# Kernel optimization log

Measured on AMD Instinct MI355X. Metric: run time of the kernel, lower is better.

The kernel has to match this reference:

```python
import jax, jax.numpy as jnp
import numpy as np

B, T, D, H, E = 4, 1024, 1024, 4096, 8
TOP_K = 2

def setup_inputs() -> dict:
    key = jax.random.key(0)
    ks = jax.random.split(key, 7)
    s = 0.02
    return {
        "x": jax.random.normal(ks[0], (B, T, D), dtype=jnp.float32),
        "gate_w": jax.random.normal(ks[1], (D, E), dtype=jnp.float32) * s,
        "gate_b": jnp.zeros((E,), dtype=jnp.float32),
        "w1": jax.random.normal(ks[2], (E, D, H), dtype=jnp.float32) * s,
        "b1": jnp.zeros((E, H), dtype=jnp.float32),
        "w2": jax.random.normal(ks[3], (E, H, D), dtype=jnp.float32) * s,
        "b2": jnp.zeros((E, D), dtype=jnp.float32),
    }

def reference(x, gate_w, gate_b, w1, b1, w2, b2):
    # gate: [B,T,E] softmax over experts
    gate_scores = jax.nn.softmax(x @ gate_w + gate_b, axis=-1)
    top_g, top_i = jax.lax.top_k(gate_scores, TOP_K)  # [B,T,K]
    # dense all-expert FFN (faithful to original: every expert on every token)
    h = jax.nn.relu(jnp.einsum("btd,edh->bteh", x, w1) + b1)   # [B,T,E,H]
    expert_out = jnp.einsum("bteh,ehd->bted", h, w2) + b2      # [B,T,E,D]
    # gather top-k expert outputs and combine with gate weights
    sel = jnp.take_along_axis(expert_out, top_i[..., None], axis=2)  # [B,T,K,D]
    return jnp.sum(top_g[..., None] * sel, axis=2)  # [B,T,D]
```

## Files before the change

### kernel.cpp

```cpp
#include <hip/hip_runtime.h>

#define MTOK   4096
#define DD     1024
#define HH     4096
#define EE     8
#define NPAIRS 8192
#define PADM   128

typedef __attribute__((ext_vector_type(8))) _Float16 half8;
typedef __attribute__((ext_vector_type(4))) _Float16 half4;
typedef __attribute__((ext_vector_type(4))) float    f32x4;

__device__ __forceinline__ void gload_lds16(const void* g, void* l) {
  __builtin_amdgcn_global_load_lds((const __attribute__((address_space(1))) void*)g,
                                   (__attribute__((address_space(3))) void*)l,
                                   16, 0, 0);
}

__global__ void k_init(int* counts) {
  if (threadIdx.x < EE) counts[threadIdx.x] = 0;
}

__global__ __launch_bounds__(256) void k_gate(
    const float* __restrict__ x, const float* __restrict__ gw,
    const float* __restrict__ gb, int* __restrict__ counts,
    int* __restrict__ topi, float* __restrict__ topg)
{
  __shared__ float W[EE][DD];
  int tid = threadIdx.x;
  for (int i = tid; i < DD*EE/4; i += 256) {
    f32x4 v = ((const f32x4*)gw)[i];
    int flat = i*4;
#pragma unroll
    for (int j = 0; j < 4; ++j) { int f = flat + j; W[f & 7][f >> 3] = v[j]; }
  }
  __syncthreads();
  int w = tid >> 6, lane = tid & 63;
  int t = blockIdx.x*4 + w;
  float acc[EE];
#pragma unroll
  for (int e = 0; e < EE; ++e) acc[e] = 0.f;
  const float* xr = x + (size_t)t*DD;
  for (int kk = 0; kk < DD/64; ++kk) {
    int k = kk*64 + lane;
    float xv = xr[k];
#pragma unroll
    for (int e = 0; e < EE; ++e) acc[e] += xv * W[e][k];
  }
#pragma unroll
  for (int off = 32; off >= 1; off >>= 1) {
#pragma unroll
    for (int e = 0; e < EE; ++e) acc[e] += __shfl_down(acc[e], off, 64);
  }
  if (lane == 0) {
#pragma unroll
    for (int e = 0; e < EE; ++e) acc[e] += gb[e];
    int i0 = 0;
#pragma unroll
    for (int e = 1; e < EE; ++e) if (acc[e] > acc[i0]) i0 = e;
    int i1 = (i0 == 0) ? 1 : 0;
#pragma unroll
    for (int e = 0; e < EE; ++e)
      if (e != i0 && e != i1 && acc[e] > acc[i1]) i1 = e;
    float m = acc[i0], s = 0.f, ex[EE];
#pragma unroll
    for (int e = 0; e < EE; ++e) { ex[e] = expf(acc[e] - m); s += ex[e]; }
    float inv = 1.f / s;
    topi[2*t] = i0;  topi[2*t+1] = i1;
    topg[2*t] = ex[i0]*inv;  topg[2*t+1] = ex[i1]*inv;
    atomicAdd(&counts[i0], 1);
    atomicAdd(&counts[i1], 1);
  }
}

__global__ void k_prefix(const int* counts, int* offs, int* cursor) {
  if (threadIdx.x == 0) {
    int s = 0;
    for (int e = 0; e < EE; ++e) { offs[e] = s; cursor[e] = s; s += counts[e]; }
    offs[EE] = s;
  }
}

__global__ void k_build(const int* __restrict__ topi, const float* __restrict__ topg,
                        int* __restrict__ cursor, int* __restrict__ tok_of,
                        float* __restrict__ gate_of, int* __restrict__ slot_of)
{
  int t = blockIdx.x*blockDim.x + threadIdx.x;
  if (t >= MTOK) return;
#pragma unroll
  for (int k = 0; k < 2; ++k) {
    int e = topi[2*t+k];
    int pos = atomicAdd(&cursor[e], 1);
    tok_of[pos]  = t;
    gate_of[pos] = topg[2*t+k];
    slot_of[2*t+k] = pos;
  }
}

__global__ __launch_bounds__(256) void k_gather(
    const float* __restrict__ x, const int* __restrict__ tok_of,
    _Float16* __restrict__ xg)
{
  int p = blockIdx.x;
  int t = tok_of[p];
  const f32x4* src = (const f32x4*)(x + (size_t)t*DD);
  half4* dst = (half4*)(xg + (size_t)p*DD);
  int i = threadIdx.x;
  f32x4 v = src[i];
  half4 h = { (_Float16)v[0], (_Float16)v[1], (_Float16)v[2], (_Float16)v[3] };
  dst[i] = h;
}

__global__ __launch_bounds__(256) void k_transpose(
    const float* __restrict__ in, _Float16* __restrict__ out, int Kd, int Nd)
{
  __shared__ _Float16 tile[64][72];
  int e = blockIdx.z;
  int n0 = blockIdx.x*64, k0 = blockIdx.y*64;
  int tid = threadIdx.x;
  int rq = tid >> 4, c4 = (tid & 15)*4;
  const float* src = in + (size_t)e*Kd*Nd;
#pragma unroll
  for (int rr = 0; rr < 4; ++rr) {
    int kr = rr*16 + rq;
    f32x4 v = *(const f32x4*)(src + (size_t)(k0+kr)*Nd + n0 + c4);
#pragma unroll
    for (int j = 0; j < 4; ++j) tile[c4+j][kr] = (_Float16)v[j];
  }
  __syncthreads();
  _Float16* dst = out + (size_t)e*Nd*Kd;
#pragma unroll
  for (int rr = 0; rr < 4; ++rr) {
    int nr = rr*16 + rq;
    half4 h;
#pragma unroll
    for (int j = 0; j < 4; ++j) h[j] = tile[nr][c4+j];
    *(half4*)(dst + (size_t)(n0+nr)*Kd + k0 + c4) = h;
  }
}

template<int EPI>
__global__ __launch_bounds__(256) void k_gemm(
    const _Float16* __restrict__ A, const _Float16* __restrict__ Bt,
    const float* __restrict__ bias, const int* __restrict__ offs,
    const int* __restrict__ counts, const float* __restrict__ gate_of,
    _Float16* __restrict__ Ch, float* __restrict__ Cf, int Kdim, int Ndim)
{
  int e = blockIdx.z;
  int cnt = counts[e];
  int m0 = blockIdx.y*128;
  if (m0 >= cnt) return;
  int n0 = blockIdx.x*128;
  int row_base = offs[e] + m0;

  __shared__ alignas(16) _Float16 lsA[128*64];
  __shared__ alignas(16) _Float16 lsB[128*64];

  int tid = threadIdx.x, w = tid >> 6, lane = tid & 63;
  int wr = w >> 1, wc = w & 1;

  f32x4 acc[4][4];
#pragma unroll
  for (int ni = 0; ni < 4; ++ni) {
    float bv = bias[(size_t)e*Ndim + n0 + wc*64 + ni*16 + (lane & 15)];
#pragma unroll
    for (int mi = 0; mi < 4; ++mi) acc[mi][ni] = (f32x4){bv, bv, bv, bv};
  }

  int arow[4], acol[4];
#pragma unroll
  for (int i = 0; i < 4; ++i) {
    int o = w*4096 + i*1024 + lane*16;
    int row = o >> 7;
    int chunk = (o >> 4) & 7;
    arow[i] = row;
    acol[i] = (chunk ^ (row & 7)) * 8;
  }

  const _Float16* Arow = A + (size_t)row_base*Kdim;
  const _Float16* Brow = Bt + ((size_t)e*Ndim + n0)*Kdim;

  for (int k0 = 0; k0 < Kdim; k0 += 64) {
#pragma unroll
    for (int i = 0; i < 4; ++i)
      gload_lds16(Arow + (size_t)arow[i]*Kdim + k0 + acol[i],
                  (char*)lsA + w*4096 + i*1024);
#pragma unroll
    for (int i = 0; i < 4; ++i)
      gload_lds16(Brow + (size_t)arow[i]*Kdim + k0 + acol[i],
                  (char*)lsB + w*4096 + i*1024);
    __syncthreads();
#pragma unroll
    for (int ks = 0; ks < 2; ++ks) {
      half8 af[4], bf[4];
#pragma unroll
      for (int mi = 0; mi < 4; ++mi) {
        int r = wr*64 + mi*16 + (lane & 15);
        int byt = (r*128 + ks*64 + ((lane >> 4) << 4)) ^ ((r & 7) << 4);
        af[mi] = *(const half8*)((const char*)lsA + byt);
      }
#pragma unroll
      for (int ni = 0; ni < 4; ++ni) {
        int r = wc*64 + ni*16 + (lane & 15);
        int byt = (r*128 + ks*64 + ((lane >> 4) << 4)) ^ ((r & 7) << 4);
        bf[ni] = *(const half8*)((const char*)lsB + byt);
      }
#pragma unroll
      for (int mi = 0; mi < 4; ++mi)
#pragma unroll
        for (int ni = 0; ni < 4; ++ni)
          acc[mi][ni] = __builtin_amdgcn_mfma_f32_16x16x32_f16(af[mi], bf[ni], acc[mi][ni], 0, 0, 0);
    }
    __syncthreads();
  }

#pragma unroll
  for (int mi = 0; mi < 4; ++mi) {
    int rl = wr*64 + mi*16 + ((lane >> 4) << 2);
#pragma unroll
    for (int ni = 0; ni < 4; ++ni) {
      int cl = n0 + wc*64 + ni*16 + (lane & 15);
#pragma unroll
      for (int r = 0; r < 4; ++r) {
        if (m0 + rl + r >= cnt) continue;
        size_t grow = (size_t)(row_base + rl + r);
        float v = acc[mi][ni][r];
        if (EPI == 0) Ch[grow*Ndim + cl] = (_Float16)fmaxf(v, 0.f);
        else          Cf[grow*Ndim + cl] = v * gate_of[grow];
      }
    }
  }
}

__global__ __launch_bounds__(256) void k_combine(
    const float* __restrict__ o2, const int* __restrict__ slot_of,
    float* __restrict__ out)
{
  int t = blockIdx.x;
  int s0 = slot_of[2*t], s1 = slot_of[2*t+1];
  const f32x4* a = (const f32x4*)(o2 + (size_t)s0*DD);
  const f32x4* b = (const f32x4*)(o2 + (size_t)s1*DD);
  f32x4* o = (f32x4*)(out + (size_t)t*DD);
  int i = threadIdx.x;
  o[i] = a[i] + b[i];
}

extern "C" void kernel_launch(void* const* d_in, const int* in_sizes, int n_in,
                              void* d_out, int out_size, void* d_ws, size_t ws_size,
                              hipStream_t stream)
{
  const float* x  = (const float*)d_in[0];
  const float* gw = (const float*)d_in[1];
  const float* gb = (const float*)d_in[2];
  const float* w1 = (const float*)d_in[3];
  const float* b1 = (const float*)d_in[4];
  const float* w2 = (const float*)d_in[5];
  const float* b2 = (const float*)d_in[6];
  float* out = (float*)d_out;
  char* ws = (char*)d_ws;

  size_t off = 0;
  auto alloc = [&](size_t b) {
    off = (off + 255) & ~(size_t)255;
    size_t o = off; off += b; return o;
  };
  int*   counts  = (int*)  (ws + alloc(EE*4));
  int*   offs    = (int*)  (ws + alloc((EE+1)*4));
  int*   cursor  = (int*)  (ws + alloc(EE*4));
  int*   topi    = (int*)  (ws + alloc((size_t)MTOK*2*4));
  float* topg    = (float*)(ws + alloc((size_t)MTOK*2*4));
  int*   tok_of  = (int*)  (ws + alloc((size_t)NPAIRS*4));
  float* gate_of = (float*)(ws + alloc((size_t)NPAIRS*4));
  int*   slot_of = (int*)  (ws + alloc((size_t)MTOK*2*4));
  _Float16* xg  = (_Float16*)(ws + alloc((size_t)(NPAIRS+PADM)*DD*2));
  _Float16* hb  = (_Float16*)(ws + alloc((size_t)(NPAIRS+PADM)*HH*2));
  _Float16* w1t = (_Float16*)(ws + alloc((size_t)EE*HH*DD*2));
  _Float16* w2t = (_Float16*)(ws + alloc((size_t)EE*DD*HH*2));
  float* o2 = (float*)w1t;

  k_init<<<1, 64, 0, stream>>>(counts);
  k_gate<<<MTOK/4, 256, 0, stream>>>(x, gw, gb, counts, topi, topg);
  k_prefix<<<1, 64, 0, stream>>>(counts, offs, cursor);
  k_build<<<MTOK/256, 256, 0, stream>>>(topi, topg, cursor, tok_of, gate_of, slot_of);
  k_gather<<<NPAIRS, 256, 0, stream>>>(x, tok_of, xg);
  k_transpose<<<dim3(HH/64, DD/64, EE), 256, 0, stream>>>(w1, w1t, DD, HH);
  k_transpose<<<dim3(DD/64, HH/64, EE), 256, 0, stream>>>(w2, w2t, HH, DD);
  k_gemm<0><<<dim3(HH/128, MTOK/128, EE), 256, 0, stream>>>(
      xg, w1t, b1, offs, counts, nullptr, hb, nullptr, DD, HH);
  k_gemm<1><<<dim3(DD/128, MTOK/128, EE), 256, 0, stream>>>(
      hb, w2t, b2, offs, counts, gate_of, nullptr, o2, HH, DD);
  k_combine<<<MTOK, 256, 0, stream>>>(o2, slot_of, out);
}
```

Measured before the change: 776.5 us.

## Double-buffer GEMM LDS, split-K second GEMM, XCD-aware block remap, staged epilogue

```diff
diff --git a/kernel.cpp b/kernel.cpp
--- a/kernel.cpp
+++ b/kernel.cpp
@@ -139,22 +139,34 @@
   }
 }
 
-template<int EPI>
+template<int EPI, int KS, int KD, int ND>
 __global__ __launch_bounds__(256) void k_gemm(
     const _Float16* __restrict__ A, const _Float16* __restrict__ Bt,
     const float* __restrict__ bias, const int* __restrict__ offs,
     const int* __restrict__ counts, const float* __restrict__ gate_of,
-    _Float16* __restrict__ Ch, float* __restrict__ Cf, int Kdim, int Ndim)
-{
-  int e = blockIdx.z;
+    _Float16* __restrict__ Ch, float* __restrict__ Cf)
+{
+  constexpr int NT = ND >> 7;
+  constexpr int MT = MTOK >> 7;
+  int total = NT * MT * EE * KS;
+  int lid = blockIdx.x;
+  int logical = (lid & 7) * (total >> 3) + (lid >> 3);
+  int n  = logical % NT;
+  int rem = logical / NT;
+  int m  = rem % MT;
+  int z  = rem / MT;
+  int e  = z / KS, ks = z % KS;
+
   int cnt = counts[e];
-  int m0 = blockIdx.y*128;
+  int m0 = m << 7;
   if (m0 >= cnt) return;
-  int n0 = blockIdx.x*128;
+  int n0 = n << 7;
   int row_base = offs[e] + m0;
-
-  __shared__ alignas(16) _Float16 lsA[128*64];
-  __shared__ alignas(16) _Float16 lsB[128*64];
+  constexpr int Kper = KD / KS;
+  int kbeg = ks * Kper;
+
+  constexpr int LSZ = (EPI == 1) ? (128*132*4) : 65536;
+  __shared__ alignas(16) char ls[LSZ];
 
   int tid = threadIdx.x, w = tid >> 6, lane = tid & 63;
   int wr = w >> 1, wc = w & 1;
@@ -162,7 +174,8 @@
   f32x4 acc[4][4];
 #pragma unroll
   for (int ni = 0; ni < 4; ++ni) {
-    float bv = bias[(size_t)e*Ndim + n0 + wc*64 + ni*16 + (lane & 15)];
+    float bv = (EPI == 0 || ks == 0)
+             ? bias[(size_t)e*ND + n0 + wc*64 + ni*16 + (lane & 15)] : 0.f;
 #pragma unroll
     for (int mi = 0; mi < 4; ++mi) acc[mi][ni] = (f32x4){bv, bv, bv, bv};
   }
@@ -177,33 +190,37 @@
     acol[i] = (chunk ^ (row & 7)) * 8;
   }
 
-  const _Float16* Arow = A + (size_t)row_base*Kdim;
-  const _Float16* Brow = Bt + ((size_t)e*Ndim + n0)*Kdim;
-
-  for (int k0 = 0; k0 < Kdim; k0 += 64) {
+  const _Float16* Arow = A + (size_t)row_base*KD + kbeg;
+  const _Float16* Brow = Bt + ((size_t)e*ND + n0)*KD + kbeg;
+
+  auto STAGE = [&](int buf, int k0) {
+    char* dA = ls + buf*16384;
+    char* dB = ls + 32768 + buf*16384;
 #pragma unroll
     for (int i = 0; i < 4; ++i)
-      gload_lds16(Arow + (size_t)arow[i]*Kdim + k0 + acol[i],
-                  (char*)lsA + w*4096 + i*1024);
+      gload_lds16(Arow + (size_t)arow[i]*KD + k0 + acol[i], dA + w*4096 + i*1024);
 #pragma unroll
     for (int i = 0; i < 4; ++i)
-      gload_lds16(Brow + (size_t)arow[i]*Kdim + k0 + acol[i],
-                  (char*)lsB + w*4096 + i*1024);
-    __syncthreads();
-#pragma unroll
-    for (int ks = 0; ks < 2; ++ks) {
+      gload_lds16(Brow + (size_t)arow[i]*KD + k0 + acol[i], dB + w*4096 + i*1024);
+  };
+
+  auto COMPUTE = [&](int buf) {
+    const char* sA = ls + buf*16384;
+    const char* sB = ls + 32768 + buf*16384;
+#pragma unroll
+    for (int ks2 = 0; ks2 < 2; ++ks2) {
       half8 af[4], bf[4];
 #pragma unroll
       for (int mi = 0; mi < 4; ++mi) {
         int r = wr*64 + mi*16 + (lane & 15);
-        int byt = (r*128 + ks*64 + ((lane >> 4) << 4)) ^ ((r & 7) << 4);
-        af[mi] = *(const half8*)((const char*)lsA + byt);
+        int byt = (r*128 + ks2*64 + ((lane >> 4) << 4)) ^ ((r & 7) << 4);
+        af[mi] = *(const half8*)(sA + byt);
       }
 #pragma unroll
       for (int ni = 0; ni < 4; ++ni) {
         int r = wc*64 + ni*16 + (lane & 15);
-        int byt = (r*128 + ks*64 + ((lane >> 4) << 4)) ^ ((r & 7) << 4);
-        bf[ni] = *(const half8*)((const char*)lsB + byt);
+        int byt = (r*128 + ks2*64 + ((lane >> 4) << 4)) ^ ((r & 7) << 4);
+        bf[ni] = *(const half8*)(sB + byt);
       }
 #pragma unroll
       for (int mi = 0; mi < 4; ++mi)
@@ -211,22 +228,67 @@
         for (int ni = 0; ni < 4; ++ni)
           acc[mi][ni] = __builtin_amdgcn_mfma_f32_16x16x32_f16(af[mi], bf[ni], acc[mi][ni], 0, 0, 0);
     }
+  };
+
+  constexpr int NTILES = Kper >> 6;
+  STAGE(0, 0);
+  __syncthreads();
+  int cur = 0;
+  for (int t = 0; t < NTILES; ++t) {
+    if (t + 1 < NTILES) STAGE(cur ^ 1, (t + 1) << 6);
+    COMPUTE(cur);
     __syncthreads();
-  }
-
-#pragma unroll
-  for (int mi = 0; mi < 4; ++mi) {
-    int rl = wr*64 + mi*16 + ((lane >> 4) << 2);
-#pragma unroll
-    for (int ni = 0; ni < 4; ++ni) {
-      int cl = n0 + wc*64 + ni*16 + (lane & 15);
-#pragma unroll
-      for (int r = 0; r < 4; ++r) {
-        if (m0 + rl + r >= cnt) continue;
-        size_t grow = (size_t)(row_base + rl + r);
-        float v = acc[mi][ni][r];
-        if (EPI == 0) Ch[grow*Ndim + cl] = (_Float16)fmaxf(v, 0.f);
-        else          Cf[grow*Ndim + cl] = v * gate_of[grow];
+    cur ^= 1;
+  }
+
+  if (EPI == 0) {
+    _Float16* T = (_Float16*)ls;
+#pragma unroll
+    for (int mi = 0; mi < 4; ++mi) {
+      int rl = wr*64 + mi*16 + ((lane >> 4) << 2);
+#pragma unroll
+      for (int ni = 0; ni < 4; ++ni) {
+        int cl = wc*64 + ni*16 + (lane & 15);
+#pragma unroll
+        for (int r = 0; r < 4; ++r)
+          T[(rl + r)*136 + cl] = (_Float16)fmaxf(acc[mi][ni][r], 0.f);
+      }
+    }
+    __syncthreads();
+#pragma unroll
+    for (int p = 0; p < 8; ++p) {
+      int flat = p*2048 + tid*8;
+      int row = flat >> 7, col = flat & 127;
+      if (m0 + row < cnt) {
+        half8 hv = *(const half8*)&T[row*136 + col];
+        *(half8*)(Ch + (size_t)(row_base + row)*ND + n0 + col) = hv;
+      }
+    }
+  } else {
+    float* T = (float*)ls;
+#pragma unroll
+    for (int mi = 0; mi < 4; ++mi) {
+      int rl = wr*64 + mi*16 + ((lane >> 4) << 2);
+#pragma unroll
+      for (int ni = 0; ni < 4; ++ni) {
+        int cl = wc*64 + ni*16 + (lane & 15);
+#pragma unroll
+        for (int r = 0; r < 4; ++r)
+          T[(rl + r)*132 + cl] = acc[mi][ni][r];
+      }
+    }
+    __syncthreads();
+    float* Cs = Cf + (size_t)ks * NPAIRS * ND;
+#pragma unroll
+    for (int p = 0; p < 16; ++p) {
+      int flat = p*1024 + tid*4;
+      int row = flat >> 7, col = flat & 127;
+      if (m0 + row < cnt) {
+        size_t grow = (size_t)(row_base + row);
+        f32x4 v = *(const f32x4*)&T[row*132 + col];
+        float g = gate_of[grow];
+        v[0] *= g; v[1] *= g; v[2] *= g; v[3] *= g;
+        *(f32x4*)(Cs + grow*ND + n0 + col) = v;
       }
     }
   }
@@ -238,11 +300,13 @@
 {
   int t = blockIdx.x;
   int s0 = slot_of[2*t], s1 = slot_of[2*t+1];
-  const f32x4* a = (const f32x4*)(o2 + (size_t)s0*DD);
-  const f32x4* b = (const f32x4*)(o2 + (size_t)s1*DD);
+  const f32x4* a0 = (const f32x4*)(o2 + (size_t)s0*DD);
+  const f32x4* a1 = (const f32x4*)(o2 + ((size_t)NPAIRS + s0)*DD);
+  const f32x4* b0 = (const f32x4*)(o2 + (size_t)s1*DD);
+  const f32x4* b1 = (const f32x4*)(o2 + ((size_t)NPAIRS + s1)*DD);
   f32x4* o = (f32x4*)(out + (size_t)t*DD);
   int i = threadIdx.x;
-  o[i] = a[i] + b[i];
+  o[i] = a0[i] + a1[i] + b0[i] + b1[i];
 }
 
 extern "C" void kernel_launch(void* const* d_in, const int* in_sizes, int n_in,
@@ -285,9 +349,9 @@
   k_gather<<<NPAIRS, 256, 0, stream>>>(x, tok_of, xg);
   k_transpose<<<dim3(HH/64, DD/64, EE), 256, 0, stream>>>(w1, w1t, DD, HH);
   k_transpose<<<dim3(DD/64, HH/64, EE), 256, 0, stream>>>(w2, w2t, HH, DD);
-  k_gemm<0><<<dim3(HH/128, MTOK/128, EE), 256, 0, stream>>>(
-      xg, w1t, b1, offs, counts, nullptr, hb, nullptr, DD, HH);
-  k_gemm<1><<<dim3(DD/128, MTOK/128, EE), 256, 0, stream>>>(
-      hb, w2t, b2, offs, counts, gate_of, nullptr, o2, HH, DD);
+  k_gemm<0,1,DD,HH><<<(HH/128)*(MTOK/128)*EE, 256, 0, stream>>>(
+      xg, w1t, b1, offs, counts, gate_of, hb, nullptr);
+  k_gemm<1,2,HH,DD><<<(DD/128)*(MTOK/128)*EE*2, 256, 0, stream>>>(
+      hb, w2t, b2, offs, counts, gate_of, nullptr, o2);
   k_combine<<<MTOK, 256, 0, stream>>>(o2, slot_of, out);
 }
```

After: 679.0 us. 12.6% less time.
